# Optimization experiments

Hardware: AMD Instinct MI355X
Metric: run time of the kernel (lower is better)

The kernel has to match this reference:

```python
import jax, jax.numpy as jnp
import numpy as np

THRESHOLD_P = 0.4  # nucleus_select default threshold_p


def setup_inputs() -> dict:
    key = jax.random.key(0)
    B, N = 512, 50257
    logits = jax.random.normal(key, (B, N), dtype=jnp.float32)
    # nucleus_select consumes softmax weights (rows sum to 1)
    weights = jax.nn.softmax(logits, axis=-1)
    return {"weights": weights}


def reference(weights):
    """Batched nucleus (top-p) selection, jit-compatible padded form.

    Returns:
      sorted_idx: (B, N) int32  -- indices of weights sorted descending
      norm_w:     (B, N) f32    -- renormalized selected weights in sorted
                                   order; positions >= k are exactly 0
      k:          (B,)   int32  -- nucleus size per sample (>= 1)
    For sample b the torch module's outputs are sorted_idx[b, :k[b]] and
    norm_w[b, :k[b]].
    """
    B, N = weights.shape
    # descending sort (values + original indices)
    sorted_idx = jnp.argsort(-weights, axis=-1)
    sorted_w = jnp.take_along_axis(weights, sorted_idx, axis=-1)
    cumsum = jnp.cumsum(sorted_w, axis=-1)
    exceeded = cumsum > THRESHOLD_P
    # first position where cumsum > p, then +1; if never exceeded, keep all N
    first = jnp.argmax(exceeded, axis=-1).astype(jnp.int32)
    k = jnp.where(jnp.any(exceeded, axis=-1), first + 1, jnp.int32(N))
    k = jnp.maximum(k, 1)
    keep = jnp.arange(N, dtype=jnp.int32)[None, :] < k[:, None]  # (B, N)
    sel_w = sorted_w * keep.astype(sorted_w.dtype)
    norm_w = sel_w / jnp.sum(sel_w, axis=-1, keepdims=True)
    return sorted_idx.astype(jnp.int32), norm_w, k
```

## Files before the change

kernel.cpp:

```cpp
#include <hip/hip_runtime.h>
#include <stdint.h>

#define B    512
#define N    50257
#define BLK  512
#define NWAVE 8
#define TILE 8192
#define CHUNK 1024
#define NGRP 16
#define THRESH 0.4f

__device__ __forceinline__ uint32_t sort_key(float w) { return ~__float_as_uint(w); }

__device__ __forceinline__ void hist_elem(uint32_t* hw0, const float w) {
    const uint32_t key = sort_key(w);
    atomicAdd(hw0 + (key & 255u), 1u);
    atomicAdd(hw0 + 256 + ((key >> 8) & 255u), 1u);
    atomicAdd(hw0 + 512 + ((key >> 16) & 255u), 1u);
    atomicAdd(hw0 + 768 + ((key >> 24) & 255u), 1u);
}

__global__ __launch_bounds__(BLK) void hist4_fast(const float* __restrict__ wts,
                                                  uint32_t* __restrict__ histWS) {
    __shared__ uint32_t hw[NWAVE][4][256];
    __shared__ uint32_t wtot[4];
    const int row = blockIdx.x;
    const size_t base = (size_t)row * N;
    const int tid = threadIdx.x;
    const int lane = tid & 63;
    const int wv = tid >> 6;

    {
        uint32_t* p = &hw[wv][0][0];
        for (int j = lane; j < 4 * 256; j += 64) p[j] = 0;
    }
    uint32_t* hw0 = &hw[wv][0][0];

    const int head = (int)((4 - (base & 3)) & 3);
    for (int i = tid; i < head; i += BLK) hist_elem(hw0, wts[base + i]);
    const int nvec = (N - head) >> 2;
    const float4* v4 = (const float4*)(wts + base + head);
    for (int iv = tid; iv < nvec; iv += BLK) {
        const float4 f = v4[iv];
        hist_elem(hw0, f.x); hist_elem(hw0, f.y);
        hist_elem(hw0, f.z); hist_elem(hw0, f.w);
    }
    for (int i = head + 4 * nvec + tid; i < N; i += BLK) hist_elem(hw0, wts[base + i]);
    __syncthreads();

    for (int p = 0; p < 4; ++p) {
        uint32_t cnt = 0;
        if (tid < 256) {
            #pragma unroll
            for (int w = 0; w < NWAVE; ++w) cnt += hw[w][p][tid];
        }
        uint32_t incl = cnt;
        #pragma unroll
        for (int o = 1; o < 64; o <<= 1) {
            const uint32_t u = __shfl_up(incl, o);
            if (lane >= o) incl += u;
        }
        if (tid < 256 && lane == 63) wtot[tid >> 6] = incl;
        __syncthreads();
        if (tid < 256) {
            uint32_t prefix = 0;
            const int w4 = tid >> 6;
            #pragma unroll
            for (int w2 = 0; w2 < 4; ++w2) if (w2 < w4) prefix += wtot[w2];
            histWS[((size_t)row * 4 + p) * 256 + tid] = prefix + incl - cnt;
        }
        __syncthreads();
    }
}

template <int SHIFT, bool FIRST, bool LAST>
__global__ __launch_bounds__(BLK, 4) void scatter_pl(const float* __restrict__ wts,
                                                     const unsigned long long* __restrict__ src,
                                                     unsigned long long* __restrict__ dst,
                                                     uint32_t* __restrict__ outIdx,
                                                     float* __restrict__ outW,
                                                     const uint32_t* __restrict__ histWS) {
    __shared__ unsigned long long stage[TILE];
    __shared__ uint32_t waveCnt[NWAVE][256];
    __shared__ uint32_t delta[256];
    __shared__ uint32_t wtot[4];

    const int row = blockIdx.x;
    const size_t base = (size_t)row * N;
    const int tid  = threadIdx.x;
    const int lane = tid & 63;
    const int wv   = tid >> 6;
    constexpr int PASS = SHIFT / 8;
    constexpr int KS = SHIFT + 16;

    uint32_t curReg = 0;
    if (tid < 256) curReg = histWS[((size_t)row * 4 + PASS) * 256 + tid];

    const int numTiles = (N + TILE - 1) / TILE;

    unsigned long long pairN[NGRP];
    {
        const int cb = wv * CHUNK;
        #pragma unroll
        for (int g = 0; g < NGRP; ++g) {
            const int i = cb + g * 64 + lane;
            pairN[g] = FIRST ? (((unsigned long long)sort_key(wts[base + i]) << 16) | (uint32_t)i)
                             : src[base + i];
        }
    }

    for (int t = 0; t < numTiles; ++t) {
        const int tbase = t * TILE;
        const int tileLen = (N - tbase < TILE) ? (N - tbase) : TILE;
        const int cbase = tbase + wv * CHUNK;
        const bool full = (tbase + TILE <= N);

        {
            uint4* z = (uint4*)&waveCnt[wv][0];
            z[lane] = make_uint4(0u, 0u, 0u, 0u);
        }
        unsigned long long pairR[NGRP];
        uint32_t posR[NGRP];
        #pragma unroll
        for (int g = 0; g < NGRP; ++g) pairR[g] = pairN[g];

        if (t + 1 < numTiles) {
            const int ncb = (t + 1) * TILE + wv * CHUNK;
            if (ncb + CHUNK <= N) {
                #pragma unroll
                for (int g = 0; g < NGRP; ++g) {
                    const int i = ncb + g * 64 + lane;
                    pairN[g] = FIRST ? (((unsigned long long)sort_key(wts[base + i]) << 16) | (uint32_t)i)
                                     : src[base + i];
                }
            } else {
                #pragma unroll
                for (int g = 0; g < NGRP; ++g) {
                    const int i = ncb + g * 64 + lane;
                    unsigned long long pair = 0;
                    if (i < N)
                        pair = FIRST ? (((unsigned long long)sort_key(wts[base + i]) << 16) | (uint32_t)i)
                                     : src[base + i];
                    pairN[g] = pair;
                }
            }
        }

        if (full) {
            #pragma unroll
            for (int g = 0; g < NGRP; ++g) {
                const uint32_t d = (uint32_t)(pairR[g] >> KS) & 255u;
                unsigned long long peers = ~0ull;
                #pragma unroll
                for (int bb = 0; bb < 8; ++bb) {
                    const unsigned long long bit = __ballot((d >> bb) & 1u);
                    peers &= ((d >> bb) & 1u) ? bit : ~bit;
                }
                const unsigned long long lower = peers & ((1ull << lane) - 1ull);
                const uint32_t cnt = waveCnt[wv][d];
                posR[g] = cnt + (uint32_t)__popcll(lower);
                if (lower == 0ull) waveCnt[wv][d] = cnt + (uint32_t)__popcll(peers);
            }
        } else {
            #pragma unroll
            for (int g = 0; g < NGRP; ++g) {
                const int i = cbase + g * 64 + lane;
                const bool valid = (i < N);
                const uint32_t d = (uint32_t)(pairR[g] >> KS) & 255u;
                unsigned long long peers = __ballot(valid);
                #pragma unroll
                for (int bb = 0; bb < 8; ++bb) {
                    const unsigned long long bit = __ballot((d >> bb) & 1u);
                    peers &= ((d >> bb) & 1u) ? bit : ~bit;
                }
                const unsigned long long lower = peers & ((1ull << lane) - 1ull);
                uint32_t cnt = 0;
                if (valid) cnt = waveCnt[wv][d];
                posR[g] = cnt + (uint32_t)__popcll(lower);
                if (valid && lower == 0ull) waveCnt[wv][d] = cnt + (uint32_t)__popcll(peers);
            }
        }
        __syncthreads();

        uint32_t run = 0;
        if (tid < 256) {
            #pragma unroll
            for (int w = 0; w < NWAVE; ++w) {
                const uint32_t c = waveCnt[w][tid];
                waveCnt[w][tid] = run;
                run += c;
            }
        }
        uint32_t incl = run;
        #pragma unroll
        for (int o = 1; o < 64; o <<= 1) {
            const uint32_t u = __shfl_up(incl, o);
            if (lane >= o) incl += u;
        }
        if (tid < 256 && lane == 63) wtot[tid >> 6] = incl;
        __syncthreads();
        if (tid < 256) {
            uint32_t prefix = 0;
            const int w4 = tid >> 6;
            #pragma unroll
            for (int w2 = 0; w2 < 4; ++w2) if (w2 < w4) prefix += wtot[w2];
            const uint32_t ts = prefix + incl - run;
            delta[tid] = curReg - ts;
            curReg += run;
            #pragma unroll
            for (int w = 0; w < NWAVE; ++w) waveCnt[w][tid] += ts;
        }
        __syncthreads();

        if (full) {
            #pragma unroll
            for (int g = 0; g < NGRP; ++g) {
                const uint32_t d = (uint32_t)(pairR[g] >> KS) & 255u;
                stage[waveCnt[wv][d] + posR[g]] = pairR[g];
            }
        } else {
            #pragma unroll
            for (int g = 0; g < NGRP; ++g) {
                const int i = cbase + g * 64 + lane;
                if (i < N) {
                    const uint32_t d = (uint32_t)(pairR[g] >> KS) & 255u;
                    stage[waveCnt[wv][d] + posR[g]] = pairR[g];
                }
            }
        }
        __syncthreads();

        const int tileLenEven = tileLen & ~1;
        for (int p0 = 2 * tid; p0 < tileLenEven; p0 += 2 * BLK) {
            const ulonglong2 two = *(const ulonglong2*)&stage[p0];
            const uint32_t d0 = (uint32_t)(two.x >> KS) & 255u;
            const uint32_t d1 = (uint32_t)(two.y >> KS) & 255u;
            const uint32_t g0 = delta[d0] + (uint32_t)p0;
            const uint32_t g1 = delta[d1] + (uint32_t)p0 + 1u;
            if (LAST) {
                outIdx[base + g0] = (uint32_t)(two.x & 0xFFFFull);
                outW[base + g0]   = __uint_as_float(~(uint32_t)(two.x >> 16));
                outIdx[base + g1] = (uint32_t)(two.y & 0xFFFFull);
                outW[base + g1]   = __uint_as_float(~(uint32_t)(two.y >> 16));
            } else {
                dst[base + g0] = two.x;
                dst[base + g1] = two.y;
            }
        }
        for (int p = tileLenEven + tid; p < tileLen; p += BLK) {
            const unsigned long long pair = stage[p];
            const uint32_t d = (uint32_t)(pair >> KS) & 255u;
            const uint32_t g = delta[d] + (uint32_t)p;
            if (LAST) {
                outIdx[base + g] = (uint32_t)(pair & 0xFFFFull);
                outW[base + g]   = __uint_as_float(~(uint32_t)(pair >> 16));
            } else {
                dst[base + g] = pair;
            }
        }
    }
}

__global__ __launch_bounds__(BLK) void finalize_row(float* __restrict__ out0,
                                                    float* __restrict__ out1,
                                                    float* __restrict__ out2) {
    __shared__ float waveSum[NWAVE];
    __shared__ int   waveFirst[NWAVE];
    __shared__ float waveCum[NWAVE];
    __shared__ int   s_k;
    __shared__ float s_total;

    const int row = blockIdx.x;
    const size_t base = (size_t)row * N;
    const int tid  = threadIdx.x;
    const int lane = tid & 63;
    const int wv   = tid >> 6;

    if (tid == 0) { s_k = -1; s_total = 0.f; }
    __syncthreads();

    float carry = 0.f;
    const int numTiles = (N + BLK - 1) / BLK;
    for (int t = 0; t < numTiles; ++t) {
        const int i = t * BLK + tid;
        const bool valid = (i < N);
        float w = valid ? out1[base + i] : 0.f;

        float s = w;
        #pragma unroll
        for (int o = 1; o < 64; o <<= 1) {
            float u = __shfl_up(s, o);
            if (lane >= o) s += u;
        }
        if (lane == 63) waveSum[wv] = s;
        __syncthreads();

        float prefix = 0.f, blockTot = 0.f;
        #pragma unroll
        for (int w2 = 0; w2 < NWAVE; ++w2) {
            float t2 = waveSum[w2];
            if (w2 < wv) prefix += t2;
            blockTot += t2;
        }
        const float cum = carry + prefix + s;

        const bool exceed = valid && (cum > THRESH);
        const unsigned long long bal = __ballot(exceed);
        const int fl = (bal == 0ull) ? 64 : (__ffsll(bal) - 1);
        if (lane == 0) waveFirst[wv] = fl;
        if (fl < 64 && lane == fl) waveCum[wv] = cum;
        __syncthreads();
        if (tid == 0) {
            for (int w2 = 0; w2 < NWAVE; ++w2) {
                if (waveFirst[w2] < 64) {
                    s_k = t * BLK + w2 * 64 + waveFirst[w2] + 1;
                    s_total = waveCum[w2];
                    break;
                }
            }
        }
        __syncthreads();
        if (s_k >= 0) break;
        carry += blockTot;
        __syncthreads();
    }

    int k = s_k;
    float total = s_total;
    if (k < 0) { k = N; total = carry; }
    const float inv = 1.0f / total;

    const uint32_t* idxU = (const uint32_t*)out0;
    const int head = (int)((4 - (base & 3)) & 3);
    const int nvec = (N - head) >> 2;
    const int vend = head + 4 * nvec;

    for (int i = tid; i < head; i += BLK) {
        const uint32_t idx = idxU[base + i];
        const float w = out1[base + i];
        out0[base + i] = (float)idx;
        out1[base + i] = (i < k) ? (w * inv) : 0.f;
    }
    const uint4*  ivp = (const uint4*)(idxU + base + head);
    float4*       o0v = (float4*)(out0 + base + head);
    float4*       o1v = (float4*)(out1 + base + head);
    for (int v = tid; v < nvec; v += BLK) {
        const uint4  iv = ivp[v];
        const float4 wv4 = o1v[v];
        const int i = head + 4 * v;
        float4 o0, o1;
        o0.x = (float)iv.x; o0.y = (float)iv.y; o0.z = (float)iv.z; o0.w = (float)iv.w;
        o1.x = (i + 0 < k) ? wv4.x * inv : 0.f;
        o1.y = (i + 1 < k) ? wv4.y * inv : 0.f;
        o1.z = (i + 2 < k) ? wv4.z * inv : 0.f;
        o1.w = (i + 3 < k) ? wv4.w * inv : 0.f;
        o0v[v] = o0;
        o1v[v] = o1;
    }
    for (int i = vend + tid; i < N; i += BLK) {
        const uint32_t idx = idxU[base + i];
        const float w = out1[base + i];
        out0[base + i] = (float)idx;
        out1[base + i] = (i < k) ? (w * inv) : 0.f;
    }
    if (tid == 0) out2[row] = (float)k;
}

#define NSUB (TILE / BLK)

template <int SHIFT, bool FIRST, bool LAST>
__global__ __launch_bounds__(BLK, 4) void scatter_tile(const float* __restrict__ wts,
                                                       const uint32_t* __restrict__ keySrc,
                                                       const uint16_t* __restrict__ idxSrc,
                                                       uint32_t* __restrict__ keyDst,
                                                       uint16_t* __restrict__ idxDst,
                                                       uint32_t* __restrict__ outIdx,
                                                       float* __restrict__ outW,
                                                       const uint32_t* __restrict__ histWS) {
    __shared__ uint32_t stageKey[TILE];
    __shared__ uint16_t stageIdx[TILE];
    __shared__ uint32_t waveCnt[NWAVE][256];
    __shared__ uint16_t subOff[NSUB][256];
    __shared__ uint32_t cursor[256];
    __shared__ uint32_t tileCnt[256];
    __shared__ uint32_t tileStart[256];
    __shared__ uint32_t scanb[256];

    const int row = blockIdx.x;
    const size_t base = (size_t)row * N;
    const int tid  = threadIdx.x;
    const int lane = tid & 63;
    const int wv   = tid >> 6;
    constexpr int PASS = SHIFT / 8;

    if (tid < 256) cursor[tid] = histWS[((size_t)row * 4 + PASS) * 256 + tid];

    const int numTiles = (N + TILE - 1) / TILE;
    for (int t = 0; t < numTiles; ++t) {
        const int tbase = t * TILE;
        const int tileLen = (N - tbase < TILE) ? (N - tbase) : TILE;

        uint32_t keyR[NSUB];
        uint32_t idxR[NSUB];
        uint32_t posR[NSUB];

        #pragma unroll
        for (int s = 0; s < NSUB; ++s) {
            for (int j = tid; j < NWAVE * 256; j += BLK) ((uint32_t*)waveCnt)[j] = 0;
            __syncthreads();

            const int i = tbase + s * BLK + tid;
            const bool valid = (i < N);
            uint32_t key = 0, idx = 0, d = 0;
            if (valid) {
                if (FIRST) { key = sort_key(wts[base + i]); idx = (uint32_t)i; }
                else       { key = keySrc[base + i]; idx = (uint32_t)idxSrc[base + i]; }
                d = (key >> SHIFT) & 255u;
            }
            keyR[s] = key;
            if (!FIRST) idxR[s] = idx;

            unsigned long long peers = __ballot(valid);
            #pragma unroll
            for (int b = 0; b < 8; ++b) {
                unsigned long long bit = __ballot(valid && ((d >> b) & 1u));
                peers &= ((d >> b) & 1u) ? bit : ~bit;
            }
            const unsigned long long lower = peers & ((1ull << lane) - 1ull);
            const uint32_t rank = (uint32_t)__popcll(lower);
            if (valid && lower == 0ull) waveCnt[wv][d] = (uint32_t)__popcll(peers);
            __syncthreads();

            if (tid < 256) {
                uint32_t x = 0;
                #pragma unroll
                for (int w = 0; w < NWAVE; ++w) {
                    uint32_t c = waveCnt[w][tid];
                    waveCnt[w][tid] = x;
                    x += c;
                }
                subOff[s][tid] = (uint16_t)x;
            }
            __syncthreads();

            posR[s] = valid ? (waveCnt[wv][d] + rank) : 0u;
            __syncthreads();
        }

        if (tid < 256) {
            uint32_t run = 0;
            #pragma unroll
            for (int s = 0; s < NSUB; ++s) {
                uint32_t c = subOff[s][tid];
                subOff[s][tid] = (uint16_t)run;
                run += c;
            }
            tileCnt[tid] = run;
            scanb[tid] = run;
        }
        __syncthreads();
        for (int off = 1; off < 256; off <<= 1) {
            uint32_t add = 0;
            if (tid < 256 && tid >= off) add = scanb[tid - off];
            __syncthreads();
            if (tid < 256) scanb[tid] += add;
            __syncthreads();
        }
        if (tid < 256) tileStart[tid] = (tid == 0) ? 0u : scanb[tid - 1];
        __syncthreads();

        #pragma unroll
        for (int s = 0; s < NSUB; ++s) {
            const int i = tbase + s * BLK + tid;
            if (i < N) {
                const uint32_t d = (keyR[s] >> SHIFT) & 255u;
                const uint32_t pos = tileStart[d] + (uint32_t)subOff[s][d] + posR[s];
                stageKey[pos] = keyR[s];
                stageIdx[pos] = (uint16_t)(FIRST ? (uint32_t)i : idxR[s]);
            }
        }
        __syncthreads();

        for (int p = tid; p < tileLen; p += BLK) {
            const uint32_t k = stageKey[p];
            const uint32_t d = (k >> SHIFT) & 255u;
            const uint32_t g = cursor[d] + (uint32_t)p - tileStart[d];
            if (LAST) {
                outIdx[base + g] = (uint32_t)stageIdx[p];
                outW[base + g]   = __uint_as_float(~k);
            } else {
                keyDst[base + g] = k;
                idxDst[base + g] = stageIdx[p];
            }
        }
        __syncthreads();
        if (tid < 256) cursor[tid] += tileCnt[tid];
        __syncthreads();
    }
}

template <int SHIFT>
__global__ __launch_bounds__(BLK) void radix_pass_fb(const float* __restrict__ wts,
                                                     const uint32_t* __restrict__ src,
                                                     uint32_t* __restrict__ dst) {
    __shared__ uint32_t hist[256];
    __shared__ uint32_t scanb[256];
    __shared__ uint32_t running[256];
    __shared__ uint32_t waveCnt[NWAVE][256];

    const int row = blockIdx.x;
    const size_t base = (size_t)row * N;
    const int tid  = threadIdx.x;
    const int lane = tid & 63;
    const int wv   = tid >> 6;

    if (tid < 256) hist[tid] = 0;
    __syncthreads();
    for (int i = tid; i < N; i += BLK) {
        uint32_t idx = (SHIFT == 0) ? (uint32_t)i : src[base + i];
        uint32_t d = (sort_key(wts[base + idx]) >> SHIFT) & 255u;
        atomicAdd(&hist[d], 1u);
    }
    __syncthreads();

    if (tid < 256) scanb[tid] = hist[tid];
    __syncthreads();
    for (int off = 1; off < 256; off <<= 1) {
        uint32_t add = 0;
        if (tid < 256 && tid >= off) add = scanb[tid - off];
        __syncthreads();
        if (tid < 256) scanb[tid] += add;
        __syncthreads();
    }
    if (tid < 256) running[tid] = (tid == 0) ? 0u : scanb[tid - 1];
    __syncthreads();

    const int numTiles = (N + BLK - 1) / BLK;
    for (int t = 0; t < numTiles; ++t) {
        for (int j = tid; j < NWAVE * 256; j += BLK) ((uint32_t*)waveCnt)[j] = 0;
        __syncthreads();

        const int i = t * BLK + tid;
        const bool valid = (i < N);
        uint32_t idx = 0, d = 0;
        if (valid) {
            idx = (SHIFT == 0) ? (uint32_t)i : src[base + i];
            d = (sort_key(wts[base + idx]) >> SHIFT) & 255u;
        }
        unsigned long long peers = __ballot(valid);
        #pragma unroll
        for (int b = 0; b < 8; ++b) {
            unsigned long long bit = __ballot(valid && ((d >> b) & 1u));
            peers &= ((d >> b) & 1u) ? bit : ~bit;
        }
        const unsigned long long lower = peers & ((1ull << lane) - 1ull);
        const uint32_t rank = (uint32_t)__popcll(lower);
        if (valid && lower == 0ull) waveCnt[wv][d] = (uint32_t)__popcll(peers);
        __syncthreads();

        if (tid < 256) {
            uint32_t s = running[tid];
            #pragma unroll
            for (int w = 0; w < NWAVE; ++w) {
                uint32_t c = waveCnt[w][tid];
                waveCnt[w][tid] = s;
                s += c;
            }
            running[tid] = s;
        }
        __syncthreads();

        if (valid) {
            uint32_t pos = waveCnt[wv][d] + rank;
            dst[base + pos] = idx;
        }
        __syncthreads();
    }
}

__global__ __launch_bounds__(BLK) void finalize_fb(const float* __restrict__ wts,
                                                   const uint32_t* __restrict__ sidx,
                                                   float* __restrict__ out0,
                                                   float* __restrict__ out1,
                                                   float* __restrict__ out2) {
    __shared__ float waveSum[NWAVE];
    __shared__ int   waveFirst[NWAVE];
    __shared__ float waveCum[NWAVE];
    __shared__ int   s_k;
    __shared__ float s_total;

    const int row = blockIdx.x;
    const size_t base = (size_t)row * N;
    const int tid  = threadIdx.x;
    const int lane = tid & 63;
    const int wv   = tid >> 6;

    if (tid == 0) { s_k = -1; s_total = 0.f; }
    __syncthreads();

    float carry = 0.f;
    const int numTiles = (N + BLK - 1) / BLK;
    for (int t = 0; t < numTiles; ++t) {
        const int i = t * BLK + tid;
        const bool valid = (i < N);
        float w = valid ? wts[base + sidx[base + i]] : 0.f;

        float s = w;
        #pragma unroll
        for (int o = 1; o < 64; o <<= 1) {
            float u = __shfl_up(s, o);
            if (lane >= o) s += u;
        }
        if (lane == 63) waveSum[wv] = s;
        __syncthreads();

        float prefix = 0.f, blockTot = 0.f;
        #pragma unroll
        for (int w2 = 0; w2 < NWAVE; ++w2) {
            float t2 = waveSum[w2];
            if (w2 < wv) prefix += t2;
            blockTot += t2;
        }
        const float cum = carry + prefix + s;

        const bool exceed = valid && (cum > THRESH);
        const unsigned long long bal = __ballot(exceed);
        const int fl = (bal == 0ull) ? 64 : (__ffsll(bal) - 1);
        if (lane == 0) waveFirst[wv] = fl;
        if (fl < 64 && lane == fl) waveCum[wv] = cum;
        __syncthreads();
        if (tid == 0) {
            for (int w2 = 0; w2 < NWAVE; ++w2) {
                if (waveFirst[w2] < 64) {
                    s_k = t * BLK + w2 * 64 + waveFirst[w2] + 1;
                    s_total = waveCum[w2];
                    break;
                }
            }
        }
        __syncthreads();
        if (s_k >= 0) break;
        carry += blockTot;
        __syncthreads();
    }

    int k = s_k;
    float total = s_total;
    if (k < 0) { k = N; total = carry; }

    for (int i = tid; i < N; i += BLK) {
        const uint32_t idx = sidx[base + i];
        const float w = wts[base + idx];
        out0[base + i] = (float)idx;
        out1[base + i] = (i < k) ? (w / total) : 0.f;
    }
    if (tid == 0) out2[row] = (float)k;
}


extern "C" void kernel_launch(void* const* d_in, const int* in_sizes, int n_in,
                              void* d_out, int out_size, void* d_ws, size_t ws_size,
                              hipStream_t stream) {
    const float* wts = (const float*)d_in[0];
    float* out0 = (float*)d_out;
    float* out1 = out0 + (size_t)B * N;
    float* out2 = out0 + 2 * (size_t)B * N;

    const size_t PAIR_BYTES = (size_t)B * N * 8;
    const size_t KEY_BYTES  = (size_t)B * N * 4;
    const size_t IDX_BYTES  = (size_t)B * N * 2;
    const size_t HIST_BYTES = (size_t)B * 4 * 256 * 4;
    const size_t WS_A = PAIR_BYTES + HIST_BYTES;
    const size_t WS_B = KEY_BYTES + IDX_BYTES + HIST_BYTES;

    dim3 g(B), b(BLK);
    if (ws_size >= WS_A) {
        uint8_t* ws = (uint8_t*)d_ws;
        unsigned long long* pairWS  = (unsigned long long*)ws;
        uint32_t*           histWS  = (uint32_t*)(ws + PAIR_BYTES);
        unsigned long long* pairOUT = (unsigned long long*)d_out;

        hist4_fast<<<g, b, 0, stream>>>(wts, histWS);
        scatter_pl<0,  true,  false><<<g, b, 0, stream>>>(wts, nullptr, pairWS, nullptr, nullptr, histWS);
        scatter_pl<8,  false, false><<<g, b, 0, stream>>>(nullptr, pairWS, pairOUT, nullptr, nullptr, histWS);
        scatter_pl<16, false, false><<<g, b, 0, stream>>>(nullptr, pairOUT, pairWS, nullptr, nullptr, histWS);
        scatter_pl<24, false, true ><<<g, b, 0, stream>>>(nullptr, pairWS, nullptr, (uint32_t*)out0, out1, histWS);
        finalize_row<<<g, b, 0, stream>>>(out0, out1, out2);
    } else if (ws_size >= WS_B) {
        uint8_t* ws = (uint8_t*)d_ws;
        uint32_t* keyWS  = (uint32_t*)ws;
        uint16_t* idxWS  = (uint16_t*)(ws + KEY_BYTES);
        uint32_t* histWS = (uint32_t*)(ws + KEY_BYTES + IDX_BYTES);
        uint32_t* keyOUT = (uint32_t*)out0;
        uint16_t* idxOUT = (uint16_t*)out1;

        hist4_fast<<<g, b, 0, stream>>>(wts, histWS);
        scatter_tile<0,  true,  false><<<g, b, 0, stream>>>(wts, nullptr, nullptr, keyWS, idxWS, nullptr, nullptr, histWS);
        scatter_tile<8,  false, false><<<g, b, 0, stream>>>(wts, keyWS, idxWS, keyOUT, idxOUT, nullptr, nullptr, histWS);
        scatter_tile<16, false, false><<<g, b, 0, stream>>>(wts, keyOUT, idxOUT, keyWS, idxWS, nullptr, nullptr, histWS);
        scatter_tile<24, false, true ><<<g, b, 0, stream>>>(wts, keyWS, idxWS, nullptr, nullptr, (uint32_t*)out0, out1, histWS);
        finalize_row<<<g, b, 0, stream>>>(out0, out1, out2);
    } else {
        uint32_t* bufA = (uint32_t*)out0;
        uint32_t* bufB = (uint32_t*)out1;
        radix_pass_fb<0 ><<<g, b, 0, stream>>>(wts, nullptr, bufA);
        radix_pass_fb<8 ><<<g, b, 0, stream>>>(wts, bufA, bufB);
        radix_pass_fb<16><<<g, b, 0, stream>>>(wts, bufB, bufA);
        radix_pass_fb<24><<<g, b, 0, stream>>>(wts, bufA, bufB);
        finalize_fb<<<g, b, 0, stream>>>(wts, bufB, out0, out1, out2);
    }
}
```

Baseline: 662.1 us.

## Shrink scatter tile and LDS footprint, reorder ranking before next-tile prefetch

Reduces the scatter kernel's tile from 8192 to 6144 elements (12 groups per wave) and stores per-wave digit counters as 16-bit values, cutting LDS and register use so the launch bound can rise from 4 to 6 blocks per CU. The ranking and scan phase now runs before the next tile's global prefetch is issued, which shortens how long the prefetched registers must stay live. Other kernels rename their counter arrays to avoid clashing with the new type. The trade-off is more tiles per row and more per-tile sync overhead, and the reordered prefetch may hide less memory latency.

```diff
diff --git a/kernel.cpp b/kernel.cpp
--- a/kernel.cpp
+++ b/kernel.cpp
@@ -5,9 +5,9 @@
 #define N    50257
 #define BLK  512
 #define NWAVE 8
-#define TILE 8192
-#define CHUNK 1024
-#define NGRP 16
+#define TILE 6144
+#define CHUNK 768
+#define NGRP 12
 #define THRESH 0.4f
 
 __device__ __forceinline__ uint32_t sort_key(float w) { return ~__float_as_uint(w); }
@@ -74,14 +74,14 @@
 }
 
 template <int SHIFT, bool FIRST, bool LAST>
-__global__ __launch_bounds__(BLK, 4) void scatter_pl(const float* __restrict__ wts,
+__global__ __launch_bounds__(BLK, 6) void scatter_pl(const float* __restrict__ wts,
                                                      const unsigned long long* __restrict__ src,
                                                      unsigned long long* __restrict__ dst,
                                                      uint32_t* __restrict__ outIdx,
                                                      float* __restrict__ outW,
                                                      const uint32_t* __restrict__ histWS) {
-    __shared__ unsigned long long stage[TILE];
-    __shared__ uint32_t waveCnt[NWAVE][256];
+    __shared__ __align__(16) unsigned long long stage[TILE];
+    __shared__ uint16_t waveCnt[NWAVE][256];
     __shared__ uint32_t delta[256];
     __shared__ uint32_t wtot[4];
 
@@ -116,13 +116,80 @@
         const bool full = (tbase + TILE <= N);
 
         {
-            uint4* z = (uint4*)&waveCnt[wv][0];
-            z[lane] = make_uint4(0u, 0u, 0u, 0u);
+            uint2* z = (uint2*)&waveCnt[wv][0];
+            z[lane] = make_uint2(0u, 0u);
         }
         unsigned long long pairR[NGRP];
         uint32_t posR[NGRP];
         #pragma unroll
         for (int g = 0; g < NGRP; ++g) pairR[g] = pairN[g];
+
+        if (full) {
+            #pragma unroll
+            for (int g = 0; g < NGRP; ++g) {
+                const uint32_t d = (uint32_t)(pairR[g] >> KS) & 255u;
+                unsigned long long peers = ~0ull;
+                #pragma unroll
+                for (int bb = 0; bb < 8; ++bb) {
+                    const unsigned long long bit = __ballot((d >> bb) & 1u);
+                    peers &= ((d >> bb) & 1u) ? bit : ~bit;
+                }
+                const unsigned long long lower = peers & ((1ull << lane) - 1ull);
+                const uint32_t cnt = (uint32_t)waveCnt[wv][d];
+                posR[g] = cnt + (uint32_t)__popcll(lower);
+                if (lower == 0ull) waveCnt[wv][d] = (uint16_t)(cnt + (uint32_t)__popcll(peers));
+            }
+        } else {
+            #pragma unroll
+            for (int g = 0; g < NGRP; ++g) {
+                const int i = cbase + g * 64 + lane;
+                const bool valid = (i < N);
+                const uint32_t d = (uint32_t)(pairR[g] >> KS) & 255u;
+                unsigned long long peers = __ballot(valid);
+                #pragma unroll
+                for (int bb = 0; bb < 8; ++bb) {
+                    const unsigned long long bit = __ballot((d >> bb) & 1u);
+                    peers &= ((d >> bb) & 1u) ? bit : ~bit;
+                }
+                const unsigned long long lower = peers & ((1ull << lane) - 1ull);
+                uint32_t cnt = 0;
+                if (valid) cnt = (uint32_t)waveCnt[wv][d];
+                posR[g] = cnt + (uint32_t)__popcll(lower);
+                if (valid && lower == 0ull) waveCnt[wv][d] = (uint16_t)(cnt + (uint32_t)__popcll(peers));
+            }
+        }
+        __syncthreads();
+
+        uint32_t run = 0;
+        if (tid < 256) {
+            #pragma unroll
+            for (int w = 0; w < NWAVE; ++w) {
+                const uint32_t c = (uint32_t)waveCnt[w][tid];
+                waveCnt[w][tid] = (uint16_t)run;
+                run += c;
+            }
+        }
+        uint32_t incl = run;
+        #pragma unroll
+        for (int o = 1; o < 64; o <<= 1) {
+            const uint32_t u = __shfl_up(incl, o);
+            if (lane >= o) incl += u;
+        }
+        if (tid < 256 && lane == 63) wtot[tid >> 6] = incl;
+        __syncthreads();
+        if (tid < 256) {
+            uint32_t prefix = 0;
+            const int w4 = tid >> 6;
+            #pragma unroll
+            for (int w2 = 0; w2 < 4; ++w2) if (w2 < w4) prefix += wtot[w2];
+            const uint32_t ts = prefix + incl - run;
+            delta[tid] = curReg - ts;
+            curReg += run;
+            #pragma unroll
+            for (int w = 0; w < NWAVE; ++w)
+                waveCnt[w][tid] = (uint16_t)((uint32_t)waveCnt[w][tid] + ts);
+        }
+        __syncthreads();
 
         if (t + 1 < numTiles) {
             const int ncb = (t + 1) * TILE + wv * CHUNK;
@@ -150,73 +217,7 @@
             #pragma unroll
             for (int g = 0; g < NGRP; ++g) {
                 const uint32_t d = (uint32_t)(pairR[g] >> KS) & 255u;
-                unsigned long long peers = ~0ull;
-                #pragma unroll
-                for (int bb = 0; bb < 8; ++bb) {
-                    const unsigned long long bit = __ballot((d >> bb) & 1u);
-                    peers &= ((d >> bb) & 1u) ? bit : ~bit;
-                }
-                const unsigned long long lower = peers & ((1ull << lane) - 1ull);
-                const uint32_t cnt = waveCnt[wv][d];
-                posR[g] = cnt + (uint32_t)__popcll(lower);
-                if (lower == 0ull) waveCnt[wv][d] = cnt + (uint32_t)__popcll(peers);
-            }
-        } else {
-            #pragma unroll
-            for (int g = 0; g < NGRP; ++g) {
-                const int i = cbase + g * 64 + lane;
-                const bool valid = (i < N);
-                const uint32_t d = (uint32_t)(pairR[g] >> KS) & 255u;
-                unsigned long long peers = __ballot(valid);
-                #pragma unroll
-                for (int bb = 0; bb < 8; ++bb) {
-                    const unsigned long long bit = __ballot((d >> bb) & 1u);
-                    peers &= ((d >> bb) & 1u) ? bit : ~bit;
-                }
-                const unsigned long long lower = peers & ((1ull << lane) - 1ull);
-                uint32_t cnt = 0;
-                if (valid) cnt = waveCnt[wv][d];
-                posR[g] = cnt + (uint32_t)__popcll(lower);
-                if (valid && lower == 0ull) waveCnt[wv][d] = cnt + (uint32_t)__popcll(peers);
-            }
-        }
-        __syncthreads();
-
-        uint32_t run = 0;
-        if (tid < 256) {
-            #pragma unroll
-            for (int w = 0; w < NWAVE; ++w) {
-                const uint32_t c = waveCnt[w][tid];
-                waveCnt[w][tid] = run;
-                run += c;
-            }
-        }
-        uint32_t incl = run;
-        #pragma unroll
-        for (int o = 1; o < 64; o <<= 1) {
-            const uint32_t u = __shfl_up(incl, o);
-            if (lane >= o) incl += u;
-        }
-        if (tid < 256 && lane == 63) wtot[tid >> 6] = incl;
-        __syncthreads();
-        if (tid < 256) {
-            uint32_t prefix = 0;
-            const int w4 = tid >> 6;
-            #pragma unroll
-            for (int w2 = 0; w2 < 4; ++w2) if (w2 < w4) prefix += wtot[w2];
-            const uint32_t ts = prefix + incl - run;
-            delta[tid] = curReg - ts;
-            curReg += run;
-            #pragma unroll
-            for (int w = 0; w < NWAVE; ++w) waveCnt[w][tid] += ts;
-        }
-        __syncthreads();
-
-        if (full) {
-            #pragma unroll
-            for (int g = 0; g < NGRP; ++g) {
-                const uint32_t d = (uint32_t)(pairR[g] >> KS) & 255u;
-                stage[waveCnt[wv][d] + posR[g]] = pairR[g];
+                stage[(uint32_t)waveCnt[wv][d] + posR[g]] = pairR[g];
             }
         } else {
             #pragma unroll
@@ -224,7 +225,7 @@
                 const int i = cbase + g * 64 + lane;
                 if (i < N) {
                     const uint32_t d = (uint32_t)(pairR[g] >> KS) & 255u;
-                    stage[waveCnt[wv][d] + posR[g]] = pairR[g];
+                    stage[(uint32_t)waveCnt[wv][d] + posR[g]] = pairR[g];
                 }
             }
         }
@@ -379,7 +380,7 @@
                                                        const uint32_t* __restrict__ histWS) {
     __shared__ uint32_t stageKey[TILE];
     __shared__ uint16_t stageIdx[TILE];
-    __shared__ uint32_t waveCnt[NWAVE][256];
+    __shared__ uint32_t waveCnt32[NWAVE][256];
     __shared__ uint16_t subOff[NSUB][256];
     __shared__ uint32_t cursor[256];
     __shared__ uint32_t tileCnt[256];
@@ -406,7 +407,7 @@
 
         #pragma unroll
         for (int s = 0; s < NSUB; ++s) {
-            for (int j = tid; j < NWAVE * 256; j += BLK) ((uint32_t*)waveCnt)[j] = 0;
+            for (int j = tid; j < NWAVE * 256; j += BLK) ((uint32_t*)waveCnt32)[j] = 0;
             __syncthreads();
 
             const int i = tbase + s * BLK + tid;
@@ -428,22 +429,22 @@
             }
             const unsigned long long lower = peers & ((1ull << lane) - 1ull);
             const uint32_t rank = (uint32_t)__popcll(lower);
-            if (valid && lower == 0ull) waveCnt[wv][d] = (uint32_t)__popcll(peers);
+            if (valid && lower == 0ull) waveCnt32[wv][d] = (uint32_t)__popcll(peers);
             __syncthreads();
 
             if (tid < 256) {
                 uint32_t x = 0;
                 #pragma unroll
                 for (int w = 0; w < NWAVE; ++w) {
-                    uint32_t c = waveCnt[w][tid];
-                    waveCnt[w][tid] = x;
+                    uint32_t c = waveCnt32[w][tid];
+                    waveCnt32[w][tid] = x;
                     x += c;
                 }
                 subOff[s][tid] = (uint16_t)x;
             }
             __syncthreads();
 
-            posR[s] = valid ? (waveCnt[wv][d] + rank) : 0u;
+            posR[s] = valid ? (waveCnt32[wv][d] + rank) : 0u;
             __syncthreads();
         }
 
@@ -506,7 +507,7 @@
     __shared__ uint32_t hist[256];
     __shared__ uint32_t scanb[256];
     __shared__ uint32_t running[256];
-    __shared__ uint32_t waveCnt[NWAVE][256];
+    __shared__ uint32_t waveCnt32[NWAVE][256];
 
     const int row = blockIdx.x;
     const size_t base = (size_t)row * N;
@@ -537,7 +538,7 @@
 
     const int numTiles = (N + BLK - 1) / BLK;
     for (int t = 0; t < numTiles; ++t) {
-        for (int j = tid; j < NWAVE * 256; j += BLK) ((uint32_t*)waveCnt)[j] = 0;
+        for (int j = tid; j < NWAVE * 256; j += BLK) ((uint32_t*)waveCnt32)[j] = 0;
         __syncthreads();
 
         const int i = t * BLK + tid;
@@ -555,15 +556,15 @@
         }
         const unsigned long long lower = peers & ((1ull << lane) - 1ull);
         const uint32_t rank = (uint32_t)__popcll(lower);
-        if (valid && lower == 0ull) waveCnt[wv][d] = (uint32_t)__popcll(peers);
+        if (valid && lower == 0ull) waveCnt32[wv][d] = (uint32_t)__popcll(peers);
         __syncthreads();
 
         if (tid < 256) {
             uint32_t s = running[tid];
             #pragma unroll
             for (int w = 0; w < NWAVE; ++w) {
-                uint32_t c = waveCnt[w][tid];
-                waveCnt[w][tid] = s;
+                uint32_t c = waveCnt32[w][tid];
+                waveCnt32[w][tid] = s;
                 s += c;
             }
             running[tid] = s;
@@ -571,7 +572,7 @@
         __syncthreads();
 
         if (valid) {
-            uint32_t pos = waveCnt[wv][d] + rank;
+            uint32_t pos = waveCnt32[wv][d] + rank;
             dst[base + pos] = idx;
         }
         __syncthreads();
```

Result: slower. 698.7 us (+5.5%).

## Store radix pairs as split key/idx arrays and delay next-tile prefetch

Applied to the files above, without the earlier changes.

The pipelined scatter kernel now reads and writes intermediate data as separate 32-bit key and 16-bit index arrays instead of packed 64-bit pairs, so each pass moves 6 bytes per element rather than 8. The older scatter_tile kernel and the packed-pair workspace path are removed, and the pipelined kernel becomes the only main path. The prefetch of the next tile moves from before the ranking step to after the scan barrier, which lowers register pressure while ranking but gives less time to hide load latency. The split 16-bit index stores may coalesce less well than the packed 64-bit stores did.

```diff
diff --git a/kernel.cpp b/kernel.cpp
--- a/kernel.cpp
+++ b/kernel.cpp
@@ -75,12 +75,14 @@
 
 template <int SHIFT, bool FIRST, bool LAST>
 __global__ __launch_bounds__(BLK, 4) void scatter_pl(const float* __restrict__ wts,
-                                                     const unsigned long long* __restrict__ src,
-                                                     unsigned long long* __restrict__ dst,
+                                                     const uint32_t* __restrict__ keySrc,
+                                                     const uint16_t* __restrict__ idxSrc,
+                                                     uint32_t* __restrict__ keyDst,
+                                                     uint16_t* __restrict__ idxDst,
                                                      uint32_t* __restrict__ outIdx,
                                                      float* __restrict__ outW,
                                                      const uint32_t* __restrict__ histWS) {
-    __shared__ unsigned long long stage[TILE];
+    __shared__ __align__(16) unsigned long long stage[TILE];
     __shared__ uint32_t waveCnt[NWAVE][256];
     __shared__ uint32_t delta[256];
     __shared__ uint32_t wtot[4];
@@ -105,7 +107,7 @@
         for (int g = 0; g < NGRP; ++g) {
             const int i = cb + g * 64 + lane;
             pairN[g] = FIRST ? (((unsigned long long)sort_key(wts[base + i]) << 16) | (uint32_t)i)
-                             : src[base + i];
+                             : (((unsigned long long)keySrc[base + i] << 16) | (uint32_t)idxSrc[base + i]);
         }
     }
 
@@ -123,28 +125,6 @@
         uint32_t posR[NGRP];
         #pragma unroll
         for (int g = 0; g < NGRP; ++g) pairR[g] = pairN[g];
-
-        if (t + 1 < numTiles) {
-            const int ncb = (t + 1) * TILE + wv * CHUNK;
-            if (ncb + CHUNK <= N) {
-                #pragma unroll
-                for (int g = 0; g < NGRP; ++g) {
-                    const int i = ncb + g * 64 + lane;
-                    pairN[g] = FIRST ? (((unsigned long long)sort_key(wts[base + i]) << 16) | (uint32_t)i)
-                                     : src[base + i];
-                }
-            } else {
-                #pragma unroll
-                for (int g = 0; g < NGRP; ++g) {
-                    const int i = ncb + g * 64 + lane;
-                    unsigned long long pair = 0;
-                    if (i < N)
-                        pair = FIRST ? (((unsigned long long)sort_key(wts[base + i]) << 16) | (uint32_t)i)
-                                     : src[base + i];
-                    pairN[g] = pair;
-                }
-            }
-        }
 
         if (full) {
             #pragma unroll
@@ -211,6 +191,28 @@
             for (int w = 0; w < NWAVE; ++w) waveCnt[w][tid] += ts;
         }
         __syncthreads();
+
+        if (t + 1 < numTiles) {
+            const int ncb = (t + 1) * TILE + wv * CHUNK;
+            if (ncb + CHUNK <= N) {
+                #pragma unroll
+                for (int g = 0; g < NGRP; ++g) {
+                    const int i = ncb + g * 64 + lane;
+                    pairN[g] = FIRST ? (((unsigned long long)sort_key(wts[base + i]) << 16) | (uint32_t)i)
+                                     : (((unsigned long long)keySrc[base + i] << 16) | (uint32_t)idxSrc[base + i]);
+                }
+            } else {
+                #pragma unroll
+                for (int g = 0; g < NGRP; ++g) {
+                    const int i = ncb + g * 64 + lane;
+                    unsigned long long pair = 0;
+                    if (i < N)
+                        pair = FIRST ? (((unsigned long long)sort_key(wts[base + i]) << 16) | (uint32_t)i)
+                                     : (((unsigned long long)keySrc[base + i] << 16) | (uint32_t)idxSrc[base + i]);
+                    pairN[g] = pair;
+                }
+            }
+        }
 
         if (full) {
             #pragma unroll
@@ -243,8 +245,10 @@
                 outIdx[base + g1] = (uint32_t)(two.y & 0xFFFFull);
                 outW[base + g1]   = __uint_as_float(~(uint32_t)(two.y >> 16));
             } else {
-                dst[base + g0] = two.x;
-                dst[base + g1] = two.y;
+                keyDst[base + g0] = (uint32_t)(two.x >> 16);
+                idxDst[base + g0] = (uint16_t)(two.x & 0xFFFFull);
+                keyDst[base + g1] = (uint32_t)(two.y >> 16);
+                idxDst[base + g1] = (uint16_t)(two.y & 0xFFFFull);
             }
         }
         for (int p = tileLenEven + tid; p < tileLen; p += BLK) {
@@ -255,7 +259,8 @@
                 outIdx[base + g] = (uint32_t)(pair & 0xFFFFull);
                 outW[base + g]   = __uint_as_float(~(uint32_t)(pair >> 16));
             } else {
-                dst[base + g] = pair;
+                keyDst[base + g] = (uint32_t)(pair >> 16);
+                idxDst[base + g] = (uint16_t)(pair & 0xFFFFull);
             }
         }
     }
@@ -366,139 +371,6 @@
     if (tid == 0) out2[row] = (float)k;
 }
 
-#define NSUB (TILE / BLK)
-
-template <int SHIFT, bool FIRST, bool LAST>
-__global__ __launch_bounds__(BLK, 4) void scatter_tile(const float* __restrict__ wts,
-                                                       const uint32_t* __restrict__ keySrc,
-                                                       const uint16_t* __restrict__ idxSrc,
-                                                       uint32_t* __restrict__ keyDst,
-                                                       uint16_t* __restrict__ idxDst,
-                                                       uint32_t* __restrict__ outIdx,
-                                                       float* __restrict__ outW,
-                                                       const uint32_t* __restrict__ histWS) {
-    __shared__ uint32_t stageKey[TILE];
-    __shared__ uint16_t stageIdx[TILE];
-    __shared__ uint32_t waveCnt[NWAVE][256];
-    __shared__ uint16_t subOff[NSUB][256];
-    __shared__ uint32_t cursor[256];
-    __shared__ uint32_t tileCnt[256];
-    __shared__ uint32_t tileStart[256];
-    __shared__ uint32_t scanb[256];
-
-    const int row = blockIdx.x;
-    const size_t base = (size_t)row * N;
-    const int tid  = threadIdx.x;
-    const int lane = tid & 63;
-    const int wv   = tid >> 6;
-    constexpr int PASS = SHIFT / 8;
-
-    if (tid < 256) cursor[tid] = histWS[((size_t)row * 4 + PASS) * 256 + tid];
-
-    const int numTiles = (N + TILE - 1) / TILE;
-    for (int t = 0; t < numTiles; ++t) {
-        const int tbase = t * TILE;
-        const int tileLen = (N - tbase < TILE) ? (N - tbase) : TILE;
-
-        uint32_t keyR[NSUB];
-        uint32_t idxR[NSUB];
-        uint32_t posR[NSUB];
-
-        #pragma unroll
-        for (int s = 0; s < NSUB; ++s) {
-            for (int j = tid; j < NWAVE * 256; j += BLK) ((uint32_t*)waveCnt)[j] = 0;
-            __syncthreads();
-
-            const int i = tbase + s * BLK + tid;
-            const bool valid = (i < N);
-            uint32_t key = 0, idx = 0, d = 0;
-            if (valid) {
-                if (FIRST) { key = sort_key(wts[base + i]); idx = (uint32_t)i; }
-                else       { key = keySrc[base + i]; idx = (uint32_t)idxSrc[base + i]; }
-                d = (key >> SHIFT) & 255u;
-            }
-            keyR[s] = key;
-            if (!FIRST) idxR[s] = idx;
-
-            unsigned long long peers = __ballot(valid);
-            #pragma unroll
-            for (int b = 0; b < 8; ++b) {
-                unsigned long long bit = __ballot(valid && ((d >> b) & 1u));
-                peers &= ((d >> b) & 1u) ? bit : ~bit;
-            }
-            const unsigned long long lower = peers & ((1ull << lane) - 1ull);
-            const uint32_t rank = (uint32_t)__popcll(lower);
-            if (valid && lower == 0ull) waveCnt[wv][d] = (uint32_t)__popcll(peers);
-            __syncthreads();
-
-            if (tid < 256) {
-                uint32_t x = 0;
-                #pragma unroll
-                for (int w = 0; w < NWAVE; ++w) {
-                    uint32_t c = waveCnt[w][tid];
-                    waveCnt[w][tid] = x;
-                    x += c;
-                }
-                subOff[s][tid] = (uint16_t)x;
-            }
-            __syncthreads();
-
-            posR[s] = valid ? (waveCnt[wv][d] + rank) : 0u;
-            __syncthreads();
-        }
-
-        if (tid < 256) {
-            uint32_t run = 0;
-            #pragma unroll
-            for (int s = 0; s < NSUB; ++s) {
-                uint32_t c = subOff[s][tid];
-                subOff[s][tid] = (uint16_t)run;
-                run += c;
-            }
-            tileCnt[tid] = run;
-            scanb[tid] = run;
-        }
-        __syncthreads();
-        for (int off = 1; off < 256; off <<= 1) {
-            uint32_t add = 0;
-            if (tid < 256 && tid >= off) add = scanb[tid - off];
-            __syncthreads();
-            if (tid < 256) scanb[tid] += add;
-            __syncthreads();
-        }
-        if (tid < 256) tileStart[tid] = (tid == 0) ? 0u : scanb[tid - 1];
-        __syncthreads();
-
-        #pragma unroll
-        for (int s = 0; s < NSUB; ++s) {
-            const int i = tbase + s * BLK + tid;
-            if (i < N) {
-                const uint32_t d = (keyR[s] >> SHIFT) & 255u;
-                const uint32_t pos = tileStart[d] + (uint32_t)subOff[s][d] + posR[s];
-                stageKey[pos] = keyR[s];
-                stageIdx[pos] = (uint16_t)(FIRST ? (uint32_t)i : idxR[s]);
-            }
-        }
-        __syncthreads();
-
-        for (int p = tid; p < tileLen; p += BLK) {
-            const uint32_t k = stageKey[p];
-            const uint32_t d = (k >> SHIFT) & 255u;
-            const uint32_t g = cursor[d] + (uint32_t)p - tileStart[d];
-            if (LAST) {
-                outIdx[base + g] = (uint32_t)stageIdx[p];
-                outW[base + g]   = __uint_as_float(~k);
-            } else {
-                keyDst[base + g] = k;
-                idxDst[base + g] = stageIdx[p];
-            }
-        }
-        __syncthreads();
-        if (tid < 256) cursor[tid] += tileCnt[tid];
-        __syncthreads();
-    }
-}
-
 template <int SHIFT>
 __global__ __launch_bounds__(BLK) void radix_pass_fb(const float* __restrict__ wts,
                                                      const uint32_t* __restrict__ src,
@@ -506,7 +378,7 @@
     __shared__ uint32_t hist[256];
     __shared__ uint32_t scanb[256];
     __shared__ uint32_t running[256];
-    __shared__ uint32_t waveCnt[NWAVE][256];
+    __shared__ uint32_t waveCnt32[NWAVE][256];
 
     const int row = blockIdx.x;
     const size_t base = (size_t)row * N;
@@ -537,7 +409,7 @@
 
     const int numTiles = (N + BLK - 1) / BLK;
     for (int t = 0; t < numTiles; ++t) {
-        for (int j = tid; j < NWAVE * 256; j += BLK) ((uint32_t*)waveCnt)[j] = 0;
+        for (int j = tid; j < NWAVE * 256; j += BLK) ((uint32_t*)waveCnt32)[j] = 0;
         __syncthreads();
 
         const int i = t * BLK + tid;
@@ -555,15 +427,15 @@
         }
         const unsigned long long lower = peers & ((1ull << lane) - 1ull);
         const uint32_t rank = (uint32_t)__popcll(lower);
-        if (valid && lower == 0ull) waveCnt[wv][d] = (uint32_t)__popcll(peers);
+        if (valid && lower == 0ull) waveCnt32[wv][d] = (uint32_t)__popcll(peers);
         __syncthreads();
 
         if (tid < 256) {
             uint32_t s = running[tid];
             #pragma unroll
             for (int w = 0; w < NWAVE; ++w) {
-                uint32_t c = waveCnt[w][tid];
-                waveCnt[w][tid] = s;
+                uint32_t c = waveCnt32[w][tid];
+                waveCnt32[w][tid] = s;
                 s += c;
             }
             running[tid] = s;
@@ -571,7 +443,7 @@
         __syncthreads();
 
         if (valid) {
-            uint32_t pos = waveCnt[wv][d] + rank;
+            uint32_t pos = waveCnt32[wv][d] + rank;
             dst[base + pos] = idx;
         }
         __syncthreads();
@@ -666,27 +538,13 @@
     float* out1 = out0 + (size_t)B * N;
     float* out2 = out0 + 2 * (size_t)B * N;
 
-    const size_t PAIR_BYTES = (size_t)B * N * 8;
     const size_t KEY_BYTES  = (size_t)B * N * 4;
     const size_t IDX_BYTES  = (size_t)B * N * 2;
     const size_t HIST_BYTES = (size_t)B * 4 * 256 * 4;
-    const size_t WS_A = PAIR_BYTES + HIST_BYTES;
-    const size_t WS_B = KEY_BYTES + IDX_BYTES + HIST_BYTES;
+    const size_t WS_NEED = KEY_BYTES + IDX_BYTES + HIST_BYTES;
 
     dim3 g(B), b(BLK);
-    if (ws_size >= WS_A) {
-        uint8_t* ws = (uint8_t*)d_ws;
-        unsigned long long* pairWS  = (unsigned long long*)ws;
-        uint32_t*           histWS  = (uint32_t*)(ws + PAIR_BYTES);
-        unsigned long long* pairOUT = (unsigned long long*)d_out;
-
-        hist4_fast<<<g, b, 0, stream>>>(wts, histWS);
-        scatter_pl<0,  true,  false><<<g, b, 0, stream>>>(wts, nullptr, pairWS, nullptr, nullptr, histWS);
-        scatter_pl<8,  false, false><<<g, b, 0, stream>>>(nullptr, pairWS, pairOUT, nullptr, nullptr, histWS);
-        scatter_pl<16, false, false><<<g, b, 0, stream>>>(nullptr, pairOUT, pairWS, nullptr, nullptr, histWS);
-        scatter_pl<24, false, true ><<<g, b, 0, stream>>>(nullptr, pairWS, nullptr, (uint32_t*)out0, out1, histWS);
-        finalize_row<<<g, b, 0, stream>>>(out0, out1, out2);
-    } else if (ws_size >= WS_B) {
+    if (ws_size >= WS_NEED) {
         uint8_t* ws = (uint8_t*)d_ws;
         uint32_t* keyWS  = (uint32_t*)ws;
         uint16_t* idxWS  = (uint16_t*)(ws + KEY_BYTES);
@@ -695,10 +553,10 @@
         uint16_t* idxOUT = (uint16_t*)out1;
 
         hist4_fast<<<g, b, 0, stream>>>(wts, histWS);
-        scatter_tile<0,  true,  false><<<g, b, 0, stream>>>(wts, nullptr, nullptr, keyWS, idxWS, nullptr, nullptr, histWS);
-        scatter_tile<8,  false, false><<<g, b, 0, stream>>>(wts, keyWS, idxWS, keyOUT, idxOUT, nullptr, nullptr, histWS);
-        scatter_tile<16, false, false><<<g, b, 0, stream>>>(wts, keyOUT, idxOUT, keyWS, idxWS, nullptr, nullptr, histWS);
-        scatter_tile<24, false, true ><<<g, b, 0, stream>>>(wts, keyWS, idxWS, nullptr, nullptr, (uint32_t*)out0, out1, histWS);
+        scatter_pl<0,  true,  false><<<g, b, 0, stream>>>(wts, nullptr, nullptr, keyWS, idxWS, nullptr, nullptr, histWS);
+        scatter_pl<8,  false, false><<<g, b, 0, stream>>>(nullptr, keyWS, idxWS, keyOUT, idxOUT, nullptr, nullptr, histWS);
+        scatter_pl<16, false, false><<<g, b, 0, stream>>>(nullptr, keyOUT, idxOUT, keyWS, idxWS, nullptr, nullptr, histWS);
+        scatter_pl<24, false, true ><<<g, b, 0, stream>>>(nullptr, keyWS, idxWS, nullptr, nullptr, (uint32_t*)out0, out1, histWS);
         finalize_row<<<g, b, 0, stream>>>(out0, out1, out2);
     } else {
         uint32_t* bufA = (uint32_t*)out0;
```

Result: faster. 636.9 us (-3.8%).
